# Kernel tuning notes

Measured on AMD Instinct MI355X. Metric: run time of the kernel, lower is better.

The kernel has to match this reference:

```python
import jax, jax.numpy as jnp
import numpy as np

H = 512
IN = 512
B = 64
T = 256
EPS = 1e-8


def _clin(x, Wr, Wi, br, bi):
    # complex linear: (Wr + i Wi)(xr + i xi) + (br + i bi); x: (B, F, 2)
    xr, xi = x[..., 0], x[..., 1]
    yr = xr @ Wr.T - xi @ Wi.T + br
    yi = xr @ Wi.T + xi @ Wr.T + bi
    return jnp.stack([yr, yi], axis=-1)


def _mod_apply(fn, z):
    # modulus nonlinearity: fn(|z|) * z / |z|
    m = jnp.sqrt(z[..., 0] ** 2 + z[..., 1] ** 2)
    s = fn(m) / (m + EPS)
    return z * s[..., None]


def _cmul(a, b):
    ar, ai = a[..., 0], a[..., 1]
    br, bi = b[..., 0], b[..., 1]
    return jnp.stack([ar * br - ai * bi, ai * br + ar * bi], axis=-1)


def _layer(x_tbf2, p):
    Wri, Wii, bri, bii, Wrh, Wih, brh, bih = p
    b = x_tbf2.shape[1]
    h0 = jnp.zeros((b, H, 2), x_tbf2.dtype)
    c0 = jnp.zeros((b, H, 2), x_tbf2.dtype)

    def step(carry, x_t):
        h, c = carry
        pre = _clin(x_t, Wri, Wii, bri, bii) + _clin(h, Wrh, Wih, brh, bih)
        gates = _mod_apply(jax.nn.sigmoid, pre[:, :3 * H])
        g_t = _mod_apply(jnp.tanh, pre[:, 3 * H:])
        i_t = gates[:, :H]
        f_t = gates[:, H:2 * H]
        o_t = gates[:, 2 * H:]
        # NOTE: cell update uses componentwise (real) multiply, matching torch.mul
        c_t = c * f_t + i_t * g_t
        # hidden update uses true complex multiply, matching self.mul
        h_t = _cmul(o_t, _mod_apply(jnp.tanh, c_t))
        return (h_t, c_t), h_t

    (hT, cT), ys = jax.lax.scan(step, (h0, c0), x_tbf2)
    return ys, hT, cT


def setup_inputs() -> dict:
    key = jax.random.key(0)
    ks = jax.random.split(key, 20)
    std = 1.0 / np.sqrt(H)

    def u(k, shape):
        return jax.random.uniform(k, shape, jnp.float32, -std, std)

    inp = {"x": jax.random.normal(ks[0], (B, T, IN, 2), jnp.float32)}
    idx = 1
    for l, fin in enumerate([IN, H]):
        for name, shape in [("i2h_Wr", (4 * H, fin)), ("i2h_Wi", (4 * H, fin)),
                            ("i2h_br", (4 * H,)), ("i2h_bi", (4 * H,)),
                            ("h2h_Wr", (4 * H, H)), ("h2h_Wi", (4 * H, H)),
                            ("h2h_br", (4 * H,)), ("h2h_bi", (4 * H,))]:
            inp[f"{name}_{l}"] = u(ks[idx], shape)
            idx += 1
    return inp


def reference(x,
              i2h_Wr_0, i2h_Wi_0, i2h_br_0, i2h_bi_0,
              h2h_Wr_0, h2h_Wi_0, h2h_br_0, h2h_bi_0,
              i2h_Wr_1, i2h_Wi_1, i2h_br_1, i2h_bi_1,
              h2h_Wr_1, h2h_Wi_1, h2h_br_1, h2h_bi_1):
    # x: (B, T, IN, 2), batch_first -> (T, B, IN, 2)
    xt = jnp.transpose(x, (1, 0, 2, 3))
    p0 = (i2h_Wr_0, i2h_Wi_0, i2h_br_0, i2h_bi_0, h2h_Wr_0, h2h_Wi_0, h2h_br_0, h2h_bi_0)
    p1 = (i2h_Wr_1, i2h_Wi_1, i2h_br_1, i2h_bi_1, h2h_Wr_1, h2h_Wi_1, h2h_br_1, h2h_bi_1)
    ys, h0, c0 = _layer(xt, p0)
    ys, h1, c1 = _layer(ys, p1)
    y = jnp.transpose(ys, (1, 0, 2, 3))  # (B, T, H, 2)
    h = jnp.stack([h0, h1], axis=0)      # (num_layers, B, H, 2)
    c = jnp.stack([c0, c1], axis=0)
    return (y, (h, c))
```

## Files before the change

### kernel.cpp

```cpp
#include <hip/hip_runtime.h>
#include <hip/hip_bf16.h>

typedef _Float16 f16;
typedef _Float16 f16x8 __attribute__((ext_vector_type(8)));
typedef float f32x4 __attribute__((ext_vector_type(4)));

#define T_ 256
#define SC 2048.0f
#define INV_SC (1.0f / 2048.0f)
#define RMASK 15
#define MFMA(A, B, C) __builtin_amdgcn_mfma_f32_16x16x32_f16(A, B, C, 0, 0, 0)


__global__ void prepack_x_kernel(const float* __restrict__ x, f16* __restrict__ X0) {
  unsigned int idx = blockIdx.x * 256 + threadIdx.x;
  int e    = idx & 7;
  int l    = (idx >> 3) & 63;
  int part = (idx >> 9) & 1;
  int ks   = (idx >> 10) & 31;
  int mt   = (idx >> 15) & 3;
  int t    = idx >> 17;
  int m = mt * 16 + (l & 15);
  int k = ks * 32 + ((l >> 4) << 3) + e;
  int cc = k >> 9, kw = k & 511;
  float v = x[(((size_t)m * T_ + t) * 512 + kw) * 2 + cc];
  f16 h = (f16)v;
  X0[idx] = part ? (f16)((v - (float)h) * SC) : h;
}

__global__ void prepack_w_kernel(const float* __restrict__ Wri, const float* __restrict__ Wii,
                                 const float* __restrict__ Wrh, const float* __restrict__ Wih,
                                 f16* __restrict__ out) {
  unsigned int idx = blockIdx.x * 256 + threadIdx.x;
  int e     = idx & 7;
  int l     = (idx >> 3) & 63;
  int ks    = (idx >> 9) & 63;
  int nt    = (idx >> 15) & 1;
  int jb    = (idx >> 16) & 127;
  int which = idx >> 23;
  int n_local = nt * 16 + (l & 15);
  int np = jb * 32 + n_local;
  int j  = np >> 3;
  int g  = (np >> 1) & 3;
  int cc = np & 1;
  int k  = ks * 32 + ((l >> 4) << 3) + e;
  int kb = k >> 9, kw = k & 511;
  size_t s = (size_t)(g * 512 + j) * 512 + kw;
  float v;
  if (cc == 0) v = (kb == 0) ? Wri[s] : (kb == 1) ? -Wii[s] : (kb == 2) ? Wrh[s] : -Wih[s];
  else         v = (kb == 0) ? Wii[s] : (kb == 1) ?  Wri[s] : (kb == 2) ? Wih[s] :  Wrh[s];
  f16 h = (f16)v;
  out[idx] = which ? (f16)((v - (float)h) * SC) : h;
}

struct PersistArgs {
  const f16* X0;
  f16* ys0;
  f16* h1;
  const f16* Wpk0;
  const f16* Wpk1;
  const float *br10, *bi10, *br20, *bi20;
  const float *br11, *bi11, *br21, *bi21;
  float* y;
  float* hout;
  float* cout;
  unsigned* flags;
};

__global__ __launch_bounds__(1024, 4) void lstm_persist(PersistArgs a) {
  extern __shared__ char smem[];
  f16* Wl = (f16*)smem;
  float* redf = (float*)(smem + 131072);
  volatile unsigned* goLds = (volatile unsigned*)(smem + 148480);

  int bid = blockIdx.x;
  int xcd = bid & 7, rr = bid >> 3;
  int lay = rr & 1;
  int jb = (rr >> 1) * 8 + xcd;
  int tid = threadIdx.x;
  int w = tid >> 6, l = tid & 63;
  int mt = w & 3, kq = w >> 2;
  int n_loc = l & 15, r0 = (l >> 4) * 4;

  int em = tid >> 2, ejl = tid & 3;
  int emt = em >> 4, eml = em & 15;
  int jg = jb * 4 + ejl;

  const f16* Wpk = lay ? a.Wpk1 : a.Wpk0;
  const f16* WhiG = Wpk + (size_t)jb * 65536;
  const f16* WloG = Wpk + 8388608 + (size_t)jb * 65536;
  for (int i = tid * 8; i < 65536; i += 8192)
    *reinterpret_cast<f16x8*>(Wl + i) = *reinterpret_cast<const f16x8*>(WhiG + i);
  if (tid == 0) *goLds = 0u;

  float bsr[4], bsi[4];
  {
    const float* br1 = lay ? a.br11 : a.br10;
    const float* bi1 = lay ? a.bi11 : a.bi10;
    const float* br2 = lay ? a.br21 : a.br20;
    const float* bi2 = lay ? a.bi21 : a.bi20;
#pragma unroll
    for (int g = 0; g < 4; ++g) {
      int nb = g * 512 + jg;
      bsr[g] = br1[nb] + br2[nb];
      bsi[g] = bi1[nb] + bi2[nb];
    }
  }
  __syncthreads();

  float c_r = 0.f, c_i = 0.f;

  for (int s = 0; s <= T_; ++s) {
    if (s > 0) {
      if (w == 0) {
        const unsigned* fp = a.flags + l * 4;
        for (;;) {
          unsigned f0 = __hip_atomic_load(fp + 0, __ATOMIC_RELAXED, __HIP_MEMORY_SCOPE_AGENT);
          unsigned f1 = __hip_atomic_load(fp + 1, __ATOMIC_RELAXED, __HIP_MEMORY_SCOPE_AGENT);
          unsigned f2 = __hip_atomic_load(fp + 2, __ATOMIC_RELAXED, __HIP_MEMORY_SCOPE_AGENT);
          unsigned f3 = __hip_atomic_load(fp + 3, __ATOMIC_RELAXED, __HIP_MEMORY_SCOPE_AGENT);
          unsigned mn = min(min(f0, f1), min(f2, f3));
          if (__all(mn >= (unsigned)s)) break;
          __builtin_amdgcn_s_sleep(1);
        }
        if (l == 0) { asm volatile("" ::: "memory"); *goLds = (unsigned)s; }
      } else {
        while (*goLds < (unsigned)s) __builtin_amdgcn_s_sleep(1);
      }
      asm volatile("" ::: "memory");
    }

    bool active = lay ? (s >= 1) : (s < T_);
    int t = lay ? (s - 1) : s;

    f32x4 comb0 = {0.f, 0.f, 0.f, 0.f}, comb1 = {0.f, 0.f, 0.f, 0.f};
    int rb0 = 0, rb1 = 0;
    if (active) {
      f32x4 acc0 = {0,0,0,0}, acc1 = {0,0,0,0}, sacc0 = {0,0,0,0}, sacc1 = {0,0,0,0};
      bool hwave = (kq >= 2);
      if (!hwave || t > 0) {
        const f16* Ab;
        if (hwave)
          Ab = (lay ? a.h1 : a.ys0) + (size_t)((t - 1) & RMASK) * 131072;
        else
          Ab = lay ? (a.ys0 + (size_t)(t & RMASK) * 131072)
                   : (a.X0 + (size_t)t * 131072);
        int ksl = (kq & 1) * 16;
        int ksg = kq * 16;
        const f16* pa = Ab + mt * 32768 + ksl * 1024 + l * 8;
        const f16* pw = Wl + ksg * 512 + l * 8;
        const f16* po = WloG + ksg * 512 + l * 8;
#pragma unroll 4
        for (int i = 0; i < 16; ++i) {
          f16x8 ah = *reinterpret_cast<const f16x8*>(pa + i * 1024);
          f16x8 al = *reinterpret_cast<const f16x8*>(pa + i * 1024 + 512);
          f16x8 w0 = *reinterpret_cast<const f16x8*>(pw + i * 512);
          f16x8 w1 = *reinterpret_cast<const f16x8*>(pw + 32768 + i * 512);
          f16x8 o0 = *reinterpret_cast<const f16x8*>(po + i * 512);
          f16x8 o1 = *reinterpret_cast<const f16x8*>(po + 32768 + i * 512);
          acc0 = MFMA(ah, w0, acc0); sacc0 = MFMA(al, w0, sacc0); sacc0 = MFMA(ah, o0, sacc0);
          acc1 = MFMA(ah, w1, acc1); sacc1 = MFMA(al, w1, sacc1); sacc1 = MFMA(ah, o1, sacc1);
        }
      }
      comb0 = acc0 + sacc0 * INV_SC;
      comb1 = acc1 + sacc1 * INV_SC;
      rb0 = (((kq >> 1) * 4 + mt) * 2 + 0) * 272 + n_loc * 17 + r0;
      rb1 = (((kq >> 1) * 4 + mt) * 2 + 1) * 272 + n_loc * 17 + r0;
      if ((kq & 1) == 0) {
#pragma unroll
        for (int q = 0; q < 4; ++q) { redf[rb0 + q] = comb0[q]; redf[rb1 + q] = comb1[q]; }
      }
    }
    __syncthreads();
    if (active && (kq & 1)) {
#pragma unroll
      for (int q = 0; q < 4; ++q) { redf[rb0 + q] += comb0[q]; redf[rb1 + q] += comb1[q]; }
    }
    __syncthreads();

    float hr = 0.f, him = 0.f, cnr = 0.f, cni = 0.f;
    if (active && tid < 256) {
      float zr[4], zi[4];
#pragma unroll
      for (int g = 0; g < 4; ++g) {
        int nl = ejl * 8 + g * 2;
        int nt_ = nl >> 4, nn = nl & 15;
        int i0 = (emt * 2 + nt_) * 272 + nn * 17 + eml;
        int i1 = ((4 + emt) * 2 + nt_) * 272 + nn * 17 + eml;
        zr[g] = redf[i0] + redf[i1] + bsr[g];
        zi[g] = redf[i0 + 17] + redf[i1 + 17] + bsi[g];
      }
      float gr[4], gi[4];
#pragma unroll
      for (int g = 0; g < 4; ++g) {
        float mag = sqrtf(zr[g] * zr[g] + zi[g] * zi[g]);
        float fn = (g < 3) ? (1.f / (1.f + __expf(-mag))) : tanhf(mag);
        float sg = fn / (mag + 1e-8f);
        gr[g] = zr[g] * sg;
        gi[g] = zi[g] * sg;
      }
      cnr = c_r * gr[1] + gr[0] * gr[3];
      cni = c_i * gi[1] + gi[0] * gi[3];
      c_r = cnr; c_i = cni;
      float mm = sqrtf(cnr * cnr + cni * cni);
      float sg = tanhf(mm) / (mm + 1e-8f);
      float dr = cnr * sg, di = cni * sg;
      hr  = gr[2] * dr - gi[2] * di;
      him = gi[2] * dr + gr[2] * di;

      f16 h0 = (f16)hr, h2 = (f16)him;
      unsigned a1 = (unsigned)__builtin_bit_cast(unsigned short, h0)
                  | ((unsigned)__builtin_bit_cast(unsigned short, (f16)((hr - (float)h0) * SC)) << 16);
      unsigned a2 = (unsigned)__builtin_bit_cast(unsigned short, h2)
                  | ((unsigned)__builtin_bit_cast(unsigned short, (f16)((him - (float)h2) * SC)) << 16);
      unsigned b1 = __shfl_xor(a1, 1, 64);
      unsigned b2 = __shfl_xor(a2, 1, 64);
      unsigned v0, v1; int kbase;
      int p = ejl >> 1;
      if ((ejl & 1) == 0) {
        v0 = (a1 & 0xffffu) | (b1 << 16);
        v1 = (a1 >> 16) | (b1 & 0xffff0000u);
        kbase = jb * 4 + 2 * p;
      } else {
        v0 = (b2 & 0xffffu) | (a2 << 16);
        v1 = (b2 >> 16) | (a2 & 0xffff0000u);
        kbase = 512 + jb * 4 + 2 * p;
      }
      f16* Yb = (lay ? a.h1 : a.ys0) + (size_t)(t & RMASK) * 131072;
      unsigned* Y32 = (unsigned*)Yb;
      int ks2 = kbase >> 5;
      int lane_h = eml + 16 * ((kbase >> 3) & 3);
      int e0 = kbase & 7;
      int idx0 = ((emt * 32 + ks2) * 2 + 0) * 512 + lane_h * 8 + e0;
      int idx1 = ((emt * 32 + ks2) * 2 + 1) * 512 + lane_h * 8 + e0;
      __hip_atomic_store(&Y32[idx0 >> 1], v0, __ATOMIC_RELAXED, __HIP_MEMORY_SCOPE_AGENT);
      __hip_atomic_store(&Y32[idx1 >> 1], v1, __ATOMIC_RELAXED, __HIP_MEMORY_SCOPE_AGENT);
    }

    asm volatile("s_waitcnt vmcnt(0)" ::: "memory");
    __syncthreads();
    if (tid == 0 && s < T_)
      __hip_atomic_store(&a.flags[bid], (unsigned)(s + 1),
                         __ATOMIC_RELAXED, __HIP_MEMORY_SCOPE_AGENT);

    if (active && tid < 256) {
      if (lay) {
        float2 yv; yv.x = hr; yv.y = him;
        *reinterpret_cast<float2*>(a.y + (((size_t)em * T_ + t) * 512 + jg) * 2) = yv;
      }
      if (t == T_ - 1) {
        float* hp = a.hout + (size_t)lay * 65536 + ((size_t)em * 512 + jg) * 2;
        hp[0] = hr; hp[1] = him;
        float* cq = a.cout + (size_t)lay * 65536 + ((size_t)em * 512 + jg) * 2;
        cq[0] = cnr; cq[1] = cni;
      }
    }
  }
}

extern "C" void kernel_launch(void* const* d_in, const int* in_sizes, int n_in,
                              void* d_out, int out_size, void* d_ws, size_t ws_size,
                              hipStream_t stream) {
  const float* x = (const float*)d_in[0];
  char* ws = (char*)d_ws;
  f16* X0   = (f16*)(ws + 0);
  f16* Wpk0 = (f16*)(ws + (size_t)67108864);
  f16* Wpk1 = (f16*)(ws + (size_t)100663296);
  f16* ys0  = (f16*)(ws + (size_t)134217728);
  f16* h1   = (f16*)(ws + (size_t)138412032);
  unsigned* flags = (unsigned*)(ws + (size_t)142606336);

  hipMemsetAsync(ws + 142606336, 0, 1024, stream);

  prepack_x_kernel<<<131072, 256, 0, stream>>>(x, X0);
  prepack_w_kernel<<<65536, 256, 0, stream>>>((const float*)d_in[1], (const float*)d_in[2],
                                              (const float*)d_in[5], (const float*)d_in[6], Wpk0);
  prepack_w_kernel<<<65536, 256, 0, stream>>>((const float*)d_in[9], (const float*)d_in[10],
                                              (const float*)d_in[13], (const float*)d_in[14], Wpk1);

  float* y = (float*)d_out;
  PersistArgs pa;
  pa.X0 = X0; pa.ys0 = ys0; pa.h1 = h1;
  pa.Wpk0 = Wpk0; pa.Wpk1 = Wpk1;
  pa.br10 = (const float*)d_in[3];  pa.bi10 = (const float*)d_in[4];
  pa.br20 = (const float*)d_in[7];  pa.bi20 = (const float*)d_in[8];
  pa.br11 = (const float*)d_in[11]; pa.bi11 = (const float*)d_in[12];
  pa.br21 = (const float*)d_in[15]; pa.bi21 = (const float*)d_in[16];
  pa.y = y; pa.hout = y + 16777216; pa.cout = y + 16777216 + 131072;
  pa.flags = flags;

  hipFuncSetAttribute((const void*)lstm_persist,
                      hipFuncAttributeMaxDynamicSharedMemorySize, 148608);
  void* kargs[] = { &pa };
  hipLaunchCooperativeKernel((const void*)lstm_persist, dim3(256), dim3(1024),
                             kargs, 148608, stream);
}
```

Baseline: 4.158 ms.

## Split persistent LSTM block sync into per-batch-group wave pipelines with LDS counters

Regroups the 16 waves so each group of four covers one 16-row batch tile, and replaces block-wide __syncthreads with per-group LDS counters using acquire/release atomics. Cross-block flags are now kept per batch group, so each group polls only the flags it depends on. Input-projection waves skip polling in layer 0. The aim is to let batch groups advance independently and to remove block-wide barrier and single-poller latency from the serial recurrence. The cost is more global flag traffic and more fragile ordering logic.

After: 10.24 ms. 2.46x slower.

```diff
diff --git a/kernel.cpp b/kernel.cpp
--- a/kernel.cpp
+++ b/kernel.cpp
@@ -67,11 +67,20 @@
   unsigned* flags;
 };
 
+__device__ __forceinline__ void lds_wait(unsigned* p, unsigned target) {
+  while (__hip_atomic_load(p, __ATOMIC_ACQUIRE, __HIP_MEMORY_SCOPE_WORKGROUP) < target)
+    __builtin_amdgcn_s_sleep(1);
+}
+__device__ __forceinline__ void lds_signal(unsigned* p, int lane) {
+  if (lane == 0)
+    __hip_atomic_fetch_add(p, 1u, __ATOMIC_RELEASE, __HIP_MEMORY_SCOPE_WORKGROUP);
+}
+
 __global__ __launch_bounds__(1024, 4) void lstm_persist(PersistArgs a) {
   extern __shared__ char smem[];
   f16* Wl = (f16*)smem;
   float* redf = (float*)(smem + 131072);
-  volatile unsigned* goLds = (volatile unsigned*)(smem + 148480);
+  unsigned* ctr = (unsigned*)(smem + 148480);
 
   int bid = blockIdx.x;
   int xcd = bid & 7, rr = bid >> 3;
@@ -79,11 +88,12 @@
   int jb = (rr >> 1) * 8 + xcd;
   int tid = threadIdx.x;
   int w = tid >> 6, l = tid & 63;
-  int mt = w & 3, kq = w >> 2;
+  int g = w >> 2, kq = w & 3;
   int n_loc = l & 15, r0 = (l >> 4) * 4;
-
-  int em = tid >> 2, ejl = tid & 3;
-  int emt = em >> 4, eml = em & 15;
+  bool xwave = (kq < 2);
+
+  int eml = l >> 2, ejl = l & 3;
+  int mG = g * 16 + eml;
   int jg = jb * 4 + ejl;
 
   const f16* Wpk = lay ? a.Wpk1 : a.Wpk0;
@@ -91,7 +101,7 @@
   const f16* WloG = Wpk + 8388608 + (size_t)jb * 65536;
   for (int i = tid * 8; i < 65536; i += 8192)
     *reinterpret_cast<f16x8*>(Wl + i) = *reinterpret_cast<const f16x8*>(WhiG + i);
-  if (tid == 0) *goLds = 0u;
+  if (tid < 4) ctr[tid] = 0u;
 
   float bsr[4], bsi[4];
   {
@@ -100,10 +110,10 @@
     const float* br2 = lay ? a.br21 : a.br20;
     const float* bi2 = lay ? a.bi21 : a.bi20;
 #pragma unroll
-    for (int g = 0; g < 4; ++g) {
-      int nb = g * 512 + jg;
-      bsr[g] = br1[nb] + br2[nb];
-      bsi[g] = bi1[nb] + bi2[nb];
+    for (int q = 0; q < 4; ++q) {
+      int nb = q * 512 + jg;
+      bsr[q] = br1[nb] + br2[nb];
+      bsi[q] = bi1[nb] + bi2[nb];
     }
   }
   __syncthreads();
@@ -111,148 +121,144 @@
   float c_r = 0.f, c_i = 0.f;
 
   for (int s = 0; s <= T_; ++s) {
-    if (s > 0) {
-      if (w == 0) {
-        const unsigned* fp = a.flags + l * 4;
-        for (;;) {
-          unsigned f0 = __hip_atomic_load(fp + 0, __ATOMIC_RELAXED, __HIP_MEMORY_SCOPE_AGENT);
-          unsigned f1 = __hip_atomic_load(fp + 1, __ATOMIC_RELAXED, __HIP_MEMORY_SCOPE_AGENT);
-          unsigned f2 = __hip_atomic_load(fp + 2, __ATOMIC_RELAXED, __HIP_MEMORY_SCOPE_AGENT);
-          unsigned f3 = __hip_atomic_load(fp + 3, __ATOMIC_RELAXED, __HIP_MEMORY_SCOPE_AGENT);
-          unsigned mn = min(min(f0, f1), min(f2, f3));
-          if (__all(mn >= (unsigned)s)) break;
-          __builtin_amdgcn_s_sleep(1);
-        }
-        if (l == 0) { asm volatile("" ::: "memory"); *goLds = (unsigned)s; }
-      } else {
-        while (*goLds < (unsigned)s) __builtin_amdgcn_s_sleep(1);
-      }
-      asm volatile("" ::: "memory");
-    }
-
     bool active = lay ? (s >= 1) : (s < T_);
     int t = lay ? (s - 1) : s;
-
-    f32x4 comb0 = {0.f, 0.f, 0.f, 0.f}, comb1 = {0.f, 0.f, 0.f, 0.f};
-    int rb0 = 0, rb1 = 0;
-    if (active) {
-      f32x4 acc0 = {0,0,0,0}, acc1 = {0,0,0,0}, sacc0 = {0,0,0,0}, sacc1 = {0,0,0,0};
-      bool hwave = (kq >= 2);
-      if (!hwave || t > 0) {
-        const f16* Ab;
-        if (hwave)
-          Ab = (lay ? a.h1 : a.ys0) + (size_t)((t - 1) & RMASK) * 131072;
-        else
-          Ab = lay ? (a.ys0 + (size_t)(t & RMASK) * 131072)
-                   : (a.X0 + (size_t)t * 131072);
-        int ksl = (kq & 1) * 16;
-        int ksg = kq * 16;
-        const f16* pa = Ab + mt * 32768 + ksl * 1024 + l * 8;
-        const f16* pw = Wl + ksg * 512 + l * 8;
-        const f16* po = WloG + ksg * 512 + l * 8;
+    unsigned base = 5u * (unsigned)s;
+
+    bool needPoll = active && (xwave ? (lay == 1 && s > 0) : (t > 0));
+    if (needPoll) {
+      const unsigned* fp = a.flags + g * 256 + l * 4;
+      for (;;) {
+        unsigned f0 = __hip_atomic_load(fp + 0, __ATOMIC_RELAXED, __HIP_MEMORY_SCOPE_AGENT);
+        unsigned f1 = __hip_atomic_load(fp + 1, __ATOMIC_RELAXED, __HIP_MEMORY_SCOPE_AGENT);
+        unsigned f2 = __hip_atomic_load(fp + 2, __ATOMIC_RELAXED, __HIP_MEMORY_SCOPE_AGENT);
+        unsigned f3 = __hip_atomic_load(fp + 3, __ATOMIC_RELAXED, __HIP_MEMORY_SCOPE_AGENT);
+        unsigned mn = min(min(f0, f1), min(f2, f3));
+        if (__all(mn >= (unsigned)s)) break;
+        __builtin_amdgcn_s_sleep(1);
+      }
+      asm volatile("" ::: "memory");
+    }
+
+    f32x4 acc0 = {0,0,0,0}, acc1 = {0,0,0,0}, sacc0 = {0,0,0,0}, sacc1 = {0,0,0,0};
+    bool doGemm = active && (xwave || t > 0);
+    if (doGemm) {
+      const f16* Ab;
+      if (xwave)
+        Ab = lay ? (a.ys0 + (size_t)(t & RMASK) * 131072)
+                 : (a.X0 + (size_t)t * 131072);
+      else
+        Ab = (lay ? a.h1 : a.ys0) + (size_t)((t - 1) & RMASK) * 131072;
+      const f16* pa = Ab + g * 32768 + (kq & 1) * 16384 + l * 8;
+      const f16* pw = Wl + kq * 8192 + l * 8;
+      const f16* po = WloG + kq * 8192 + l * 8;
 #pragma unroll 4
-        for (int i = 0; i < 16; ++i) {
-          f16x8 ah = *reinterpret_cast<const f16x8*>(pa + i * 1024);
-          f16x8 al = *reinterpret_cast<const f16x8*>(pa + i * 1024 + 512);
-          f16x8 w0 = *reinterpret_cast<const f16x8*>(pw + i * 512);
-          f16x8 w1 = *reinterpret_cast<const f16x8*>(pw + 32768 + i * 512);
-          f16x8 o0 = *reinterpret_cast<const f16x8*>(po + i * 512);
-          f16x8 o1 = *reinterpret_cast<const f16x8*>(po + 32768 + i * 512);
-          acc0 = MFMA(ah, w0, acc0); sacc0 = MFMA(al, w0, sacc0); sacc0 = MFMA(ah, o0, sacc0);
-          acc1 = MFMA(ah, w1, acc1); sacc1 = MFMA(al, w1, sacc1); sacc1 = MFMA(ah, o1, sacc1);
-        }
-      }
-      comb0 = acc0 + sacc0 * INV_SC;
-      comb1 = acc1 + sacc1 * INV_SC;
-      rb0 = (((kq >> 1) * 4 + mt) * 2 + 0) * 272 + n_loc * 17 + r0;
-      rb1 = (((kq >> 1) * 4 + mt) * 2 + 1) * 272 + n_loc * 17 + r0;
-      if ((kq & 1) == 0) {
-#pragma unroll
-        for (int q = 0; q < 4; ++q) { redf[rb0 + q] = comb0[q]; redf[rb1 + q] = comb1[q]; }
-      }
-    }
-    __syncthreads();
-    if (active && (kq & 1)) {
+      for (int i = 0; i < 16; ++i) {
+        f16x8 ah = *reinterpret_cast<const f16x8*>(pa + i * 1024);
+        f16x8 al = *reinterpret_cast<const f16x8*>(pa + i * 1024 + 512);
+        f16x8 w0 = *reinterpret_cast<const f16x8*>(pw + i * 512);
+        f16x8 w1 = *reinterpret_cast<const f16x8*>(pw + 32768 + i * 512);
+        f16x8 o0 = *reinterpret_cast<const f16x8*>(po + i * 512);
+        f16x8 o1 = *reinterpret_cast<const f16x8*>(po + 32768 + i * 512);
+        acc0 = MFMA(ah, w0, acc0); sacc0 = MFMA(al, w0, sacc0); sacc0 = MFMA(ah, o0, sacc0);
+        acc1 = MFMA(ah, w1, acc1); sacc1 = MFMA(al, w1, sacc1); sacc1 = MFMA(ah, o1, sacc1);
+      }
+    }
+    f32x4 comb0 = acc0 + sacc0 * INV_SC;
+    f32x4 comb1 = acc1 + sacc1 * INV_SC;
+
+    int rb0 = ((g * 2 + (kq >> 1)) * 2 + 0) * 272 + n_loc * 17 + r0;
+    int rb1 = rb0 + 272;
+    if ((kq & 1) == 0) {
+      lds_wait(&ctr[g], base);
+#pragma unroll
+      for (int q = 0; q < 4; ++q) { redf[rb0 + q] = comb0[q]; redf[rb1 + q] = comb1[q]; }
+      lds_signal(&ctr[g], l);
+    } else {
+      lds_wait(&ctr[g], base + 2);
 #pragma unroll
       for (int q = 0; q < 4; ++q) { redf[rb0 + q] += comb0[q]; redf[rb1 + q] += comb1[q]; }
-    }
-    __syncthreads();
-
-    float hr = 0.f, him = 0.f, cnr = 0.f, cni = 0.f;
-    if (active && tid < 256) {
+      lds_signal(&ctr[g], l);
+    }
+
+    if (kq == 0) {
+      lds_wait(&ctr[g], base + 4);
+      float hr = 0.f, him = 0.f, cnr = 0.f, cni = 0.f;
       float zr[4], zi[4];
-#pragma unroll
-      for (int g = 0; g < 4; ++g) {
-        int nl = ejl * 8 + g * 2;
-        int nt_ = nl >> 4, nn = nl & 15;
-        int i0 = (emt * 2 + nt_) * 272 + nn * 17 + eml;
-        int i1 = ((4 + emt) * 2 + nt_) * 272 + nn * 17 + eml;
-        zr[g] = redf[i0] + redf[i1] + bsr[g];
-        zi[g] = redf[i0 + 17] + redf[i1 + 17] + bsi[g];
-      }
-      float gr[4], gi[4];
-#pragma unroll
-      for (int g = 0; g < 4; ++g) {
-        float mag = sqrtf(zr[g] * zr[g] + zi[g] * zi[g]);
-        float fn = (g < 3) ? (1.f / (1.f + __expf(-mag))) : tanhf(mag);
-        float sg = fn / (mag + 1e-8f);
-        gr[g] = zr[g] * sg;
-        gi[g] = zi[g] * sg;
-      }
-      cnr = c_r * gr[1] + gr[0] * gr[3];
-      cni = c_i * gi[1] + gi[0] * gi[3];
-      c_r = cnr; c_i = cni;
-      float mm = sqrtf(cnr * cnr + cni * cni);
-      float sg = tanhf(mm) / (mm + 1e-8f);
-      float dr = cnr * sg, di = cni * sg;
-      hr  = gr[2] * dr - gi[2] * di;
-      him = gi[2] * dr + gr[2] * di;
-
-      f16 h0 = (f16)hr, h2 = (f16)him;
-      unsigned a1 = (unsigned)__builtin_bit_cast(unsigned short, h0)
-                  | ((unsigned)__builtin_bit_cast(unsigned short, (f16)((hr - (float)h0) * SC)) << 16);
-      unsigned a2 = (unsigned)__builtin_bit_cast(unsigned short, h2)
-                  | ((unsigned)__builtin_bit_cast(unsigned short, (f16)((him - (float)h2) * SC)) << 16);
-      unsigned b1 = __shfl_xor(a1, 1, 64);
-      unsigned b2 = __shfl_xor(a2, 1, 64);
-      unsigned v0, v1; int kbase;
-      int p = ejl >> 1;
-      if ((ejl & 1) == 0) {
-        v0 = (a1 & 0xffffu) | (b1 << 16);
-        v1 = (a1 >> 16) | (b1 & 0xffff0000u);
-        kbase = jb * 4 + 2 * p;
-      } else {
-        v0 = (b2 & 0xffffu) | (a2 << 16);
-        v1 = (b2 >> 16) | (a2 & 0xffff0000u);
-        kbase = 512 + jb * 4 + 2 * p;
-      }
-      f16* Yb = (lay ? a.h1 : a.ys0) + (size_t)(t & RMASK) * 131072;
-      unsigned* Y32 = (unsigned*)Yb;
-      int ks2 = kbase >> 5;
-      int lane_h = eml + 16 * ((kbase >> 3) & 3);
-      int e0 = kbase & 7;
-      int idx0 = ((emt * 32 + ks2) * 2 + 0) * 512 + lane_h * 8 + e0;
-      int idx1 = ((emt * 32 + ks2) * 2 + 1) * 512 + lane_h * 8 + e0;
-      __hip_atomic_store(&Y32[idx0 >> 1], v0, __ATOMIC_RELAXED, __HIP_MEMORY_SCOPE_AGENT);
-      __hip_atomic_store(&Y32[idx1 >> 1], v1, __ATOMIC_RELAXED, __HIP_MEMORY_SCOPE_AGENT);
-    }
-
-    asm volatile("s_waitcnt vmcnt(0)" ::: "memory");
-    __syncthreads();
-    if (tid == 0 && s < T_)
-      __hip_atomic_store(&a.flags[bid], (unsigned)(s + 1),
-                         __ATOMIC_RELAXED, __HIP_MEMORY_SCOPE_AGENT);
-
-    if (active && tid < 256) {
-      if (lay) {
-        float2 yv; yv.x = hr; yv.y = him;
-        *reinterpret_cast<float2*>(a.y + (((size_t)em * T_ + t) * 512 + jg) * 2) = yv;
-      }
-      if (t == T_ - 1) {
-        float* hp = a.hout + (size_t)lay * 65536 + ((size_t)em * 512 + jg) * 2;
-        hp[0] = hr; hp[1] = him;
-        float* cq = a.cout + (size_t)lay * 65536 + ((size_t)em * 512 + jg) * 2;
-        cq[0] = cnr; cq[1] = cni;
+      if (active) {
+#pragma unroll
+        for (int q = 0; q < 4; ++q) {
+          int nl = ejl * 8 + q * 2;
+          int nt_ = nl >> 4, nn = nl & 15;
+          int i0 = ((g * 2 + 0) * 2 + nt_) * 272 + nn * 17 + eml;
+          int i1 = ((g * 2 + 1) * 2 + nt_) * 272 + nn * 17 + eml;
+          zr[q] = redf[i0] + redf[i1] + bsr[q];
+          zi[q] = redf[i0 + 17] + redf[i1 + 17] + bsi[q];
+        }
+      }
+      lds_signal(&ctr[g], l);
+      if (active) {
+        float gr[4], gi[4];
+#pragma unroll
+        for (int q = 0; q < 4; ++q) {
+          float mag = sqrtf(zr[q] * zr[q] + zi[q] * zi[q]);
+          float fn = (q < 3) ? (1.f / (1.f + __expf(-mag))) : tanhf(mag);
+          float sg = fn / (mag + 1e-8f);
+          gr[q] = zr[q] * sg;
+          gi[q] = zi[q] * sg;
+        }
+        cnr = c_r * gr[1] + gr[0] * gr[3];
+        cni = c_i * gi[1] + gi[0] * gi[3];
+        c_r = cnr; c_i = cni;
+        float mm = sqrtf(cnr * cnr + cni * cni);
+        float sg = tanhf(mm) / (mm + 1e-8f);
+        float dr = cnr * sg, di = cni * sg;
+        hr  = gr[2] * dr - gi[2] * di;
+        him = gi[2] * dr + gr[2] * di;
+
+        f16 h0 = (f16)hr, h2 = (f16)him;
+        unsigned a1 = (unsigned)__builtin_bit_cast(unsigned short, h0)
+                    | ((unsigned)__builtin_bit_cast(unsigned short, (f16)((hr - (float)h0) * SC)) << 16);
+        unsigned a2 = (unsigned)__builtin_bit_cast(unsigned short, h2)
+                    | ((unsigned)__builtin_bit_cast(unsigned short, (f16)((him - (float)h2) * SC)) << 16);
+        unsigned b1 = __shfl_xor(a1, 1, 64);
+        unsigned b2 = __shfl_xor(a2, 1, 64);
+        unsigned v0, v1; int kbase;
+        int p = ejl >> 1;
+        if ((ejl & 1) == 0) {
+          v0 = (a1 & 0xffffu) | (b1 << 16);
+          v1 = (a1 >> 16) | (b1 & 0xffff0000u);
+          kbase = jb * 4 + 2 * p;
+        } else {
+          v0 = (b2 & 0xffffu) | (a2 << 16);
+          v1 = (b2 >> 16) | (a2 & 0xffff0000u);
+          kbase = 512 + jb * 4 + 2 * p;
+        }
+        f16* Yb = (lay ? a.h1 : a.ys0) + (size_t)(t & RMASK) * 131072;
+        unsigned* Y32 = (unsigned*)Yb;
+        int ks2 = kbase >> 5;
+        int lane_h = eml + 16 * ((kbase >> 3) & 3);
+        int e0 = kbase & 7;
+        int idx0 = ((g * 32 + ks2) * 2 + 0) * 512 + lane_h * 8 + e0;
+        int idx1 = ((g * 32 + ks2) * 2 + 1) * 512 + lane_h * 8 + e0;
+        __hip_atomic_store(&Y32[idx0 >> 1], v0, __ATOMIC_RELAXED, __HIP_MEMORY_SCOPE_AGENT);
+        __hip_atomic_store(&Y32[idx1 >> 1], v1, __ATOMIC_RELAXED, __HIP_MEMORY_SCOPE_AGENT);
+      }
+      asm volatile("s_waitcnt vmcnt(0)" ::: "memory");
+      if (l == 0 && s < T_)
+        __hip_atomic_store(&a.flags[g * 256 + bid], (unsigned)(s + 1),
+                           __ATOMIC_RELAXED, __HIP_MEMORY_SCOPE_AGENT);
+      if (active) {
+        if (lay) {
+          float2 yv; yv.x = hr; yv.y = him;
+          *reinterpret_cast<float2*>(a.y + (((size_t)mG * T_ + t) * 512 + jg) * 2) = yv;
+        }
+        if (t == T_ - 1) {
+          float* hp = a.hout + (size_t)lay * 65536 + ((size_t)mG * 512 + jg) * 2;
+          hp[0] = hr; hp[1] = him;
+          float* cq = a.cout + (size_t)lay * 65536 + ((size_t)mG * 512 + jg) * 2;
+          cq[0] = cnr; cq[1] = cni;
+        }
       }
     }
   }
@@ -270,7 +276,7 @@
   f16* h1   = (f16*)(ws + (size_t)138412032);
   unsigned* flags = (unsigned*)(ws + (size_t)142606336);
 
-  hipMemsetAsync(ws + 142606336, 0, 1024, stream);
+  hipMemsetAsync(ws + 142606336, 0, 4096, stream);
 
   prepack_x_kernel<<<131072, 256, 0, stream>>>(x, X0);
   prepack_w_kernel<<<65536, 256, 0, stream>>>((const float*)d_in[1], (const float*)d_in[2],
```

## Use FP8 MFMA for the weight-residual correction term in split-precision GEMM

Applied to the files above, without the earlier changes.

The third correction product (activation high part times weight low residual) now runs on fp8 operands: weight residuals are packed as fp8, and fp8 copies of the input and hidden/ys activations are produced and stored alongside the f16 versions. The goal is to halve global traffic for the residual weights streamed each step and to use the faster fp8 MFMA. The cost is an extra prepack kernel, extra fp8 stores with shuffles in the recurrent epilogue, and reduced accuracy of the correction term.

Result: slower. 4.535 ms (+9.1%).

```diff
diff --git a/kernel.cpp b/kernel.cpp
--- a/kernel.cpp
+++ b/kernel.cpp
@@ -4,12 +4,19 @@
 typedef _Float16 f16;
 typedef _Float16 f16x8 __attribute__((ext_vector_type(8)));
 typedef float f32x4 __attribute__((ext_vector_type(4)));
+typedef unsigned char u8;
 
 #define T_ 256
 #define SC 2048.0f
 #define INV_SC (1.0f / 2048.0f)
 #define RMASK 15
-#define MFMA(A, B, C) __builtin_amdgcn_mfma_f32_16x16x32_f16(A, B, C, 0, 0, 0)
+#define MFMA(A, B, C)  __builtin_amdgcn_mfma_f32_16x16x32_f16(A, B, C, 0, 0, 0)
+#define MFMA8(A, B, C) __builtin_amdgcn_mfma_f32_16x16x32_fp8_fp8(A, B, C, 0, 0, 0)
+
+__device__ __forceinline__ u8 f2fp8(float v) {
+  int r = __builtin_amdgcn_cvt_pk_fp8_f32(v, 0.f, 0, false);
+  return (u8)(r & 0xff);
+}
 
 
 __global__ void prepack_x_kernel(const float* __restrict__ x, f16* __restrict__ X0) {
@@ -28,16 +35,29 @@
   X0[idx] = part ? (f16)((v - (float)h) * SC) : h;
 }
 
+__global__ void prepack_x8_kernel(const float* __restrict__ x, u8* __restrict__ X8) {
+  unsigned int idx = blockIdx.x * 256 + threadIdx.x;
+  int e  = idx & 7;
+  int l  = (idx >> 3) & 63;
+  int ks = (idx >> 9) & 31;
+  int mt = (idx >> 14) & 3;
+  int t  = idx >> 16;
+  int m = mt * 16 + (l & 15);
+  int k = ks * 32 + ((l >> 4) << 3) + e;
+  int cc = k >> 9, kw = k & 511;
+  float v = x[(((size_t)m * T_ + t) * 512 + kw) * 2 + cc];
+  X8[idx] = f2fp8(v);
+}
+
 __global__ void prepack_w_kernel(const float* __restrict__ Wri, const float* __restrict__ Wii,
                                  const float* __restrict__ Wrh, const float* __restrict__ Wih,
-                                 f16* __restrict__ out) {
+                                 f16* __restrict__ hi, u8* __restrict__ lo8) {
   unsigned int idx = blockIdx.x * 256 + threadIdx.x;
-  int e     = idx & 7;
-  int l     = (idx >> 3) & 63;
-  int ks    = (idx >> 9) & 63;
-  int nt    = (idx >> 15) & 1;
-  int jb    = (idx >> 16) & 127;
-  int which = idx >> 23;
+  int e  = idx & 7;
+  int l  = (idx >> 3) & 63;
+  int ks = (idx >> 9) & 63;
+  int nt = (idx >> 15) & 1;
+  int jb = idx >> 16;
   int n_local = nt * 16 + (l & 15);
   int np = jb * 32 + n_local;
   int j  = np >> 3;
@@ -50,15 +70,21 @@
   if (cc == 0) v = (kb == 0) ? Wri[s] : (kb == 1) ? -Wii[s] : (kb == 2) ? Wrh[s] : -Wih[s];
   else         v = (kb == 0) ? Wii[s] : (kb == 1) ?  Wri[s] : (kb == 2) ? Wih[s] :  Wrh[s];
   f16 h = (f16)v;
-  out[idx] = which ? (f16)((v - (float)h) * SC) : h;
+  hi[idx] = h;
+  lo8[idx] = f2fp8((v - (float)h) * SC);
 }
 
 struct PersistArgs {
   const f16* X0;
+  const u8*  X8;
   f16* ys0;
   f16* h1;
-  const f16* Wpk0;
-  const f16* Wpk1;
+  u8*  ys08;
+  u8*  h18;
+  const f16* Whi0;
+  const f16* Whi1;
+  const u8*  Wlo80;
+  const u8*  Wlo81;
   const float *br10, *bi10, *br20, *bi20;
   const float *br11, *bi11, *br21, *bi21;
   float* y;
@@ -86,9 +112,8 @@
   int emt = em >> 4, eml = em & 15;
   int jg = jb * 4 + ejl;
 
-  const f16* Wpk = lay ? a.Wpk1 : a.Wpk0;
-  const f16* WhiG = Wpk + (size_t)jb * 65536;
-  const f16* WloG = Wpk + 8388608 + (size_t)jb * 65536;
+  const f16* WhiG = (lay ? a.Whi1 : a.Whi0) + (size_t)jb * 65536;
+  const u8*  Wlo8G = (lay ? a.Wlo81 : a.Wlo80) + (size_t)jb * 65536;
   for (int i = tid * 8; i < 65536; i += 8192)
     *reinterpret_cast<f16x8*>(Wl + i) = *reinterpret_cast<const f16x8*>(WhiG + i);
   if (tid == 0) *goLds = 0u;
@@ -139,27 +164,31 @@
       f32x4 acc0 = {0,0,0,0}, acc1 = {0,0,0,0}, sacc0 = {0,0,0,0}, sacc1 = {0,0,0,0};
       bool hwave = (kq >= 2);
       if (!hwave || t > 0) {
-        const f16* Ab;
-        if (hwave)
-          Ab = (lay ? a.h1 : a.ys0) + (size_t)((t - 1) & RMASK) * 131072;
-        else
-          Ab = lay ? (a.ys0 + (size_t)(t & RMASK) * 131072)
-                   : (a.X0 + (size_t)t * 131072);
+        const f16* Ab; const u8* Ab8;
+        if (!hwave) {
+          Ab  = lay ? (a.ys0 + (size_t)(t & RMASK) * 131072) : (a.X0 + (size_t)t * 131072);
+          Ab8 = lay ? (a.ys08 + (size_t)(t & RMASK) * 65536) : (a.X8 + (size_t)t * 65536);
+        } else {
+          Ab  = (lay ? a.h1  : a.ys0)  + (size_t)((t - 1) & RMASK) * 131072;
+          Ab8 = (lay ? a.h18 : a.ys08) + (size_t)((t - 1) & RMASK) * 65536;
+        }
         int ksl = (kq & 1) * 16;
         int ksg = kq * 16;
-        const f16* pa = Ab + mt * 32768 + ksl * 1024 + l * 8;
-        const f16* pw = Wl + ksg * 512 + l * 8;
-        const f16* po = WloG + ksg * 512 + l * 8;
+        const f16* pa  = Ab + mt * 32768 + ksl * 1024 + l * 8;
+        const u8*  pa8 = Ab8 + mt * 16384 + ksl * 512 + l * 8;
+        const f16* pw  = Wl + ksg * 512 + l * 8;
+        const u8*  po8 = Wlo8G + ksg * 512 + l * 8;
 #pragma unroll 4
         for (int i = 0; i < 16; ++i) {
           f16x8 ah = *reinterpret_cast<const f16x8*>(pa + i * 1024);
           f16x8 al = *reinterpret_cast<const f16x8*>(pa + i * 1024 + 512);
           f16x8 w0 = *reinterpret_cast<const f16x8*>(pw + i * 512);
           f16x8 w1 = *reinterpret_cast<const f16x8*>(pw + 32768 + i * 512);
-          f16x8 o0 = *reinterpret_cast<const f16x8*>(po + i * 512);
-          f16x8 o1 = *reinterpret_cast<const f16x8*>(po + 32768 + i * 512);
-          acc0 = MFMA(ah, w0, acc0); sacc0 = MFMA(al, w0, sacc0); sacc0 = MFMA(ah, o0, sacc0);
-          acc1 = MFMA(ah, w1, acc1); sacc1 = MFMA(al, w1, sacc1); sacc1 = MFMA(ah, o1, sacc1);
+          long a8  = *reinterpret_cast<const long*>(pa8 + i * 512);
+          long o0  = *reinterpret_cast<const long*>(po8 + i * 512);
+          long o1  = *reinterpret_cast<const long*>(po8 + 32768 + i * 512);
+          acc0 = MFMA(ah, w0, acc0); sacc0 = MFMA(al, w0, sacc0); sacc0 = MFMA8(a8, o0, sacc0);
+          acc1 = MFMA(ah, w1, acc1); sacc1 = MFMA(al, w1, sacc1); sacc1 = MFMA8(a8, o1, sacc1);
         }
       }
       comb0 = acc0 + sacc0 * INV_SC;
@@ -235,6 +264,23 @@
       int idx1 = ((emt * 32 + ks2) * 2 + 1) * 512 + lane_h * 8 + e0;
       __hip_atomic_store(&Y32[idx0 >> 1], v0, __ATOMIC_RELAXED, __HIP_MEMORY_SCOPE_AGENT);
       __hip_atomic_store(&Y32[idx1 >> 1], v1, __ATOMIC_RELAXED, __HIP_MEMORY_SCOPE_AGENT);
+
+      unsigned wr8 = ((unsigned)f2fp8(hr))  << (8 * ejl);
+      unsigned wi8 = ((unsigned)f2fp8(him)) << (8 * ejl);
+      wr8 |= __shfl_xor(wr8, 1, 64); wr8 |= __shfl_xor(wr8, 2, 64);
+      wi8 |= __shfl_xor(wi8, 1, 64); wi8 |= __shfl_xor(wi8, 2, 64);
+      u8* Yb8 = (lay ? a.h18 : a.ys08) + (size_t)(t & RMASK) * 65536;
+      unsigned* Y832 = (unsigned*)Yb8;
+      int lane_r = eml + 16 * ((jb >> 1) & 3);
+      int e08 = (jb & 1) * 4;
+      int ksr8 = jb >> 3;
+      if (ejl == 0) {
+        int b = (((emt * 32 + ksr8) * 64 + lane_r) * 8 + e08) >> 2;
+        __hip_atomic_store(&Y832[b], wr8, __ATOMIC_RELAXED, __HIP_MEMORY_SCOPE_AGENT);
+      } else if (ejl == 1) {
+        int b = (((emt * 32 + 16 + ksr8) * 64 + lane_r) * 8 + e08) >> 2;
+        __hip_atomic_store(&Y832[b], wi8, __ATOMIC_RELAXED, __HIP_MEMORY_SCOPE_AGENT);
+      }
     }
 
     asm volatile("s_waitcnt vmcnt(0)" ::: "memory");
@@ -263,25 +309,33 @@
                               hipStream_t stream) {
   const float* x = (const float*)d_in[0];
   char* ws = (char*)d_ws;
-  f16* X0   = (f16*)(ws + 0);
-  f16* Wpk0 = (f16*)(ws + (size_t)67108864);
-  f16* Wpk1 = (f16*)(ws + (size_t)100663296);
-  f16* ys0  = (f16*)(ws + (size_t)134217728);
-  f16* h1   = (f16*)(ws + (size_t)138412032);
-  unsigned* flags = (unsigned*)(ws + (size_t)142606336);
-
-  hipMemsetAsync(ws + 142606336, 0, 1024, stream);
+  f16* X0    = (f16*)(ws + 0);
+  u8*  X8    = (u8*) (ws + (size_t)67108864);
+  f16* Whi0  = (f16*)(ws + (size_t)83886080);
+  f16* Whi1  = (f16*)(ws + (size_t)100663296);
+  u8*  Wlo80 = (u8*) (ws + (size_t)117440512);
+  u8*  Wlo81 = (u8*) (ws + (size_t)125829120);
+  f16* ys0   = (f16*)(ws + (size_t)134217728);
+  f16* h1    = (f16*)(ws + (size_t)138412032);
+  u8*  ys08  = (u8*) (ws + (size_t)142606336);
+  u8*  h18   = (u8*) (ws + (size_t)143654912);
+  unsigned* flags = (unsigned*)(ws + (size_t)144703488);
+
+  hipMemsetAsync(ws + 144703488, 0, 1024, stream);
 
   prepack_x_kernel<<<131072, 256, 0, stream>>>(x, X0);
-  prepack_w_kernel<<<65536, 256, 0, stream>>>((const float*)d_in[1], (const float*)d_in[2],
-                                              (const float*)d_in[5], (const float*)d_in[6], Wpk0);
-  prepack_w_kernel<<<65536, 256, 0, stream>>>((const float*)d_in[9], (const float*)d_in[10],
-                                              (const float*)d_in[13], (const float*)d_in[14], Wpk1);
+  prepack_x8_kernel<<<65536, 256, 0, stream>>>(x, X8);
+  prepack_w_kernel<<<32768, 256, 0, stream>>>((const float*)d_in[1], (const float*)d_in[2],
+                                              (const float*)d_in[5], (const float*)d_in[6],
+                                              Whi0, Wlo80);
+  prepack_w_kernel<<<32768, 256, 0, stream>>>((const float*)d_in[9], (const float*)d_in[10],
+                                              (const float*)d_in[13], (const float*)d_in[14],
+                                              Whi1, Wlo81);
 
   float* y = (float*)d_out;
   PersistArgs pa;
-  pa.X0 = X0; pa.ys0 = ys0; pa.h1 = h1;
-  pa.Wpk0 = Wpk0; pa.Wpk1 = Wpk1;
+  pa.X0 = X0; pa.X8 = X8; pa.ys0 = ys0; pa.h1 = h1; pa.ys08 = ys08; pa.h18 = h18;
+  pa.Whi0 = Whi0; pa.Whi1 = Whi1; pa.Wlo80 = Wlo80; pa.Wlo81 = Wlo81;
   pa.br10 = (const float*)d_in[3];  pa.bi10 = (const float*)d_in[4];
   pa.br20 = (const float*)d_in[7];  pa.bi20 = (const float*)d_in[8];
   pa.br11 = (const float*)d_in[11]; pa.bi11 = (const float*)d_in[12];
```

## Precompute next step's input projection off the recurrent critical path

Applied to the files above, without the earlier changes.

Carrier waves (kq>=2) now compute the input-to-hidden MFMA contribution for the next timestep right after publishing the step flag, so it overlaps the barrier wait. After the wait, all four k-quarter wave groups split only the recurrent h-projection, halving per-wave serial work on the critical path. Layer 1 now lags layer 0 by two stages instead of one, adding one extra pipeline stage. Layer 1's early X projection reads the ys0 ring slot from one stage earlier, which relies on ordering through the flag protocol.

New measurement: 3.985 ms (median of 2 runs). -4.2%, faster.

```diff
diff --git a/kernel.cpp b/kernel.cpp
--- a/kernel.cpp
+++ b/kernel.cpp
@@ -9,7 +9,8 @@
 #define SC 2048.0f
 #define INV_SC (1.0f / 2048.0f)
 #define RMASK 15
-#define MFMA(A, B, C) __builtin_amdgcn_mfma_f32_16x16x32_f16(A, B, C, 0, 0, 0)
+#define NSTAGE 258
+#define MFMA(A, B, C)  __builtin_amdgcn_mfma_f32_16x16x32_f16(A, B, C, 0, 0, 0)
 
 
 __global__ void prepack_x_kernel(const float* __restrict__ x, f16* __restrict__ X0) {
@@ -81,6 +82,7 @@
   int w = tid >> 6, l = tid & 63;
   int mt = w & 3, kq = w >> 2;
   int n_loc = l & 15, r0 = (l >> 4) * 4;
+  bool carrier = (kq >= 2);
 
   int em = tid >> 2, ejl = tid & 3;
   int emt = em >> 4, eml = em & 15;
@@ -108,9 +110,33 @@
   }
   __syncthreads();
 
+  const f32x4 z4 = {0.f, 0.f, 0.f, 0.f};
+  f32x4 xm0 = z4, xs0 = z4, xm1 = z4, xs1 = z4;
+
+  if (carrier && lay == 0) {
+    int ksl = (kq - 2) * 16;
+    const f16* pa = a.X0 + mt * 32768 + ksl * 1024 + l * 8;
+    const f16* pw = Wl + ksl * 512 + l * 8;
+    const f16* po = WloG + ksl * 512 + l * 8;
+#pragma unroll 4
+    for (int i = 0; i < 16; ++i) {
+      f16x8 ah = *reinterpret_cast<const f16x8*>(pa + i * 1024);
+      f16x8 al = *reinterpret_cast<const f16x8*>(pa + i * 1024 + 512);
+      f16x8 w0 = *reinterpret_cast<const f16x8*>(pw + i * 512);
+      f16x8 w1 = *reinterpret_cast<const f16x8*>(pw + 32768 + i * 512);
+      f16x8 o0 = *reinterpret_cast<const f16x8*>(po + i * 512);
+      f16x8 o1 = *reinterpret_cast<const f16x8*>(po + 32768 + i * 512);
+      xm0 = MFMA(ah, w0, xm0); xs0 = MFMA(al, w0, xs0); xs0 = MFMA(ah, o0, xs0);
+      xm1 = MFMA(ah, w1, xm1); xs1 = MFMA(al, w1, xs1); xs1 = MFMA(ah, o1, xs1);
+    }
+  }
+
   float c_r = 0.f, c_i = 0.f;
 
-  for (int s = 0; s <= T_; ++s) {
+  for (int s = 0; s < NSTAGE; ++s) {
+    bool active = lay ? (s >= 2) : (s < T_);
+    int t = lay ? (s - 2) : s;
+
     if (s > 0) {
       if (w == 0) {
         const unsigned* fp = a.flags + l * 4;
@@ -130,28 +156,22 @@
       asm volatile("" ::: "memory");
     }
 
-    bool active = lay ? (s >= 1) : (s < T_);
-    int t = lay ? (s - 1) : s;
-
-    f32x4 comb0 = {0.f, 0.f, 0.f, 0.f}, comb1 = {0.f, 0.f, 0.f, 0.f};
+    f32x4 comb0 = z4, comb1 = z4;
     int rb0 = 0, rb1 = 0;
     if (active) {
-      f32x4 acc0 = {0,0,0,0}, acc1 = {0,0,0,0}, sacc0 = {0,0,0,0}, sacc1 = {0,0,0,0};
-      bool hwave = (kq >= 2);
-      if (!hwave || t > 0) {
-        const f16* Ab;
-        if (hwave)
-          Ab = (lay ? a.h1 : a.ys0) + (size_t)((t - 1) & RMASK) * 131072;
-        else
-          Ab = lay ? (a.ys0 + (size_t)(t & RMASK) * 131072)
-                   : (a.X0 + (size_t)t * 131072);
-        int ksl = (kq & 1) * 16;
-        int ksg = kq * 16;
+      f32x4 acc0  = carrier ? xm0 : z4;
+      f32x4 sacc0 = carrier ? xs0 : z4;
+      f32x4 acc1  = carrier ? xm1 : z4;
+      f32x4 sacc1 = carrier ? xs1 : z4;
+      if (t > 0) {
+        const f16* Ab = (lay ? a.h1 : a.ys0) + (size_t)((t - 1) & RMASK) * 131072;
+        int ksl = kq * 8;
+        int ksg = 32 + kq * 8;
         const f16* pa = Ab + mt * 32768 + ksl * 1024 + l * 8;
         const f16* pw = Wl + ksg * 512 + l * 8;
         const f16* po = WloG + ksg * 512 + l * 8;
-#pragma unroll 4
-        for (int i = 0; i < 16; ++i) {
+#pragma unroll
+        for (int i = 0; i < 8; ++i) {
           f16x8 ah = *reinterpret_cast<const f16x8*>(pa + i * 1024);
           f16x8 al = *reinterpret_cast<const f16x8*>(pa + i * 1024 + 512);
           f16x8 w0 = *reinterpret_cast<const f16x8*>(pw + i * 512);
@@ -239,9 +259,34 @@
 
     asm volatile("s_waitcnt vmcnt(0)" ::: "memory");
     __syncthreads();
-    if (tid == 0 && s < T_)
+    if (tid == 0 && s + 1 < NSTAGE)
       __hip_atomic_store(&a.flags[bid], (unsigned)(s + 1),
                          __ATOMIC_RELAXED, __HIP_MEMORY_SCOPE_AGENT);
+
+    if (carrier) {
+      xm0 = z4; xs0 = z4; xm1 = z4; xs1 = z4;
+      bool nextAct = lay ? (s + 1 >= 2 && s + 1 < NSTAGE) : (s + 1 < T_);
+      if (nextAct) {
+        int tn = lay ? (s - 1) : (s + 1);
+        const f16* Ab = lay ? (a.ys0 + (size_t)(tn & RMASK) * 131072)
+                            : (a.X0 + (size_t)tn * 131072);
+        int ksl = (kq - 2) * 16;
+        const f16* pa = Ab + mt * 32768 + ksl * 1024 + l * 8;
+        const f16* pw = Wl + ksl * 512 + l * 8;
+        const f16* po = WloG + ksl * 512 + l * 8;
+#pragma unroll 4
+        for (int i = 0; i < 16; ++i) {
+          f16x8 ah = *reinterpret_cast<const f16x8*>(pa + i * 1024);
+          f16x8 al = *reinterpret_cast<const f16x8*>(pa + i * 1024 + 512);
+          f16x8 w0 = *reinterpret_cast<const f16x8*>(pw + i * 512);
+          f16x8 w1 = *reinterpret_cast<const f16x8*>(pw + 32768 + i * 512);
+          f16x8 o0 = *reinterpret_cast<const f16x8*>(po + i * 512);
+          f16x8 o1 = *reinterpret_cast<const f16x8*>(po + 32768 + i * 512);
+          xm0 = MFMA(ah, w0, xm0); xs0 = MFMA(al, w0, xs0); xs0 = MFMA(ah, o0, xs0);
+          xm1 = MFMA(ah, w1, xm1); xs1 = MFMA(al, w1, xs1); xs1 = MFMA(ah, o1, xs1);
+        }
+      }
+    }
 
     if (active && tid < 256) {
       if (lay) {
```
